# Kernel optimization log

Measured on AMD Instinct MI355X. Metric: run time of the kernel, lower is better.

## Reference

```python
import jax, jax.numpy as jnp
import numpy as np

N = 8192       # nodes
E = 131072     # edges
R = 4          # relations
IN_EMBD = 64   # per-feature embedding dim -> node feat = 6*64 = 384
H1 = 256       # layer_embd
D = 128        # out_embd; layer2 outputs 2*D
VOCABS = [35, 10, 5, 7, 5, 5]


def setup_inputs() -> dict:
    key = jax.random.key(0)
    ks = jax.random.split(key, 20)
    inp = {}
    inp['x'] = jax.random.randint(ks[0], (N, 6), 0, 5)
    inp['edge_index'] = jax.random.randint(ks[1], (2, E), 0, N)
    inp['edge_type'] = jax.random.randint(ks[2], (E,), 0, R)
    for i, v in enumerate(VOCABS):
        inp[f'emb{i}'] = jax.random.normal(ks[3 + i], (v, IN_EMBD), jnp.float32) * 0.1
    inp['W1'] = jax.random.normal(ks[10], (R, 6 * IN_EMBD, H1), jnp.float32) * 0.05
    inp['root1'] = jax.random.normal(ks[11], (6 * IN_EMBD, H1), jnp.float32) * 0.05
    inp['b1'] = jnp.zeros((H1,), jnp.float32)
    inp['W2'] = jax.random.normal(ks[12], (R, H1, 2 * D), jnp.float32) * 0.05
    inp['root2'] = jax.random.normal(ks[13], (H1, 2 * D), jnp.float32) * 0.05
    inp['b2'] = jnp.zeros((2 * D,), jnp.float32)
    return inp


def _rgcn(h, W, root, b, src, dst, edge_type):
    # RGCNConv (PyG semantics): out_i = root h_i + b + sum_r mean_{j in N_r(i)} W_r h_j
    out = h @ root + b
    for r in range(R):
        hr = h @ W[r]                                   # [N, out]
        m = (edge_type == r).astype(h.dtype)            # [E]
        s = jax.ops.segment_sum(hr[src] * m[:, None], dst, num_segments=N)
        c = jax.ops.segment_sum(m, dst, num_segments=N)
        out = out + s / jnp.clip(c, 1.0)[:, None]
    return out


def reference(x, edge_index, edge_type, emb0, emb1, emb2, emb3, emb4, emb5,
              W1, root1, b1, W2, root2, b2):
    embs = [emb0, emb1, emb2, emb3, emb4, emb5]
    x_ = jnp.concatenate([embs[i][x[:, i]] for i in range(6)], axis=1)  # [N, 384]
    src, dst = edge_index[0], edge_index[1]
    h1 = jax.nn.sigmoid(_rgcn(x_, W1, root1, b1, src, dst, edge_type))
    h2 = jax.nn.sigmoid(_rgcn(h1, W2, root2, b2, src, dst, edge_type))
    mu, logvar = h2[:, :D], h2[:, D:]
    std = jnp.exp(0.5 * logvar)
    eps = jax.random.normal(jax.random.key(42), std.shape, std.dtype)
    Z = eps * std + mu                                   # reparametrize
    A_hat = jax.nn.sigmoid(Z @ Z.T)                      # [N, N]
    A = jnp.zeros((N, N), jnp.float32).at[src, dst].set(1.0)
    return A, A_hat, mu, logvar
```

## Files before the change

### kernel.cpp

```cpp
#include <hip/hip_runtime.h>
#include <hip/hip_bf16.h>
#include <cstdint>
#include <cstddef>

#define N_NODES 8192
#define NE      131072
#define NR      4
#define NC      1280
#define SLOTS   96

typedef __attribute__((ext_vector_type(8))) short bf16x8;
typedef __attribute__((ext_vector_type(4))) float f32x4;

__device__ __forceinline__ float sigmoidf_(float x) {
  return 1.0f / (1.0f + __expf(-x));
}

__device__ __forceinline__ ushort f2b(float v) {
  __hip_bfloat16 h = __float2bfloat16(v);
  return *(ushort*)&h;
}
__device__ __forceinline__ float b2f(ushort u) {
  __hip_bfloat16 h = *(__hip_bfloat16*)&u;
  return __bfloat162float(h);
}
__device__ __forceinline__ void split2(float v, ushort& hi, ushort& lo) {
  hi = f2b(v);
  lo = f2b(v - b2f(hi));
}
__device__ __forceinline__ bf16x8 pack8(float4 a, float4 b) {
  bf16x8 r;
  r[0] = (short)f2b(a.x); r[1] = (short)f2b(a.y); r[2] = (short)f2b(a.z); r[3] = (short)f2b(a.w);
  r[4] = (short)f2b(b.x); r[5] = (short)f2b(b.y); r[6] = (short)f2b(b.z); r[7] = (short)f2b(b.w);
  return r;
}

__global__ __launch_bounds__(256) void k_pack_all(
    const float* __restrict__ r1, const float* __restrict__ W1,
    const float* __restrict__ r2, const float* __restrict__ W2,
    ushort* __restrict__ B1t, ushort* __restrict__ B2thi, ushort* __restrict__ B2tlo) {
  __shared__ ushort sh[64][66];
  __shared__ ushort sl[64][66];
  int b = blockIdx.x;
  int layer, K, kt, nt, seg;
  const float *srcR, *srcW;
  if (b < 120) { layer = 1; K = 384; int t = b;       seg = t / 24; t %= 24; kt = t / 4; nt = t % 4; srcR = r1; srcW = W1; }
  else         { layer = 2; K = 256; int t = b - 120; seg = t / 16; t %= 16; kt = t / 4; nt = t % 4; srcR = r2; srcW = W2; }
  int k0 = kt * 64, n0 = nt * 64;
  int tid = threadIdx.x;
#pragma unroll
  for (int it = 0; it < 16; ++it) {
    int idx = it * 256 + tid;
    int kl = idx >> 6, nl = idx & 63;
    int kg = k0 + kl, c = n0 + nl;
    float v = (seg == 0) ? srcR[(size_t)kg * 256 + c]
                         : srcW[((size_t)(seg - 1) * K + kg) * 256 + c];
    ushort h, l; split2(v, h, l);
    sh[kl][nl] = h;
    sl[kl][nl] = l;
  }
  __syncthreads();
#pragma unroll
  for (int it = 0; it < 16; ++it) {
    int idx = it * 256 + tid;
    int nl = idx >> 6, kl = idx & 63;
    size_t o = (size_t)(seg * 256 + n0 + nl) * K + k0 + kl;
    if (layer == 1) {
      B1t[o] = sh[kl][nl];
    } else {
      B2thi[o] = sh[kl][nl];
      B2tlo[o] = sl[kl][nl];
    }
  }
}

__global__ void k_fill2(const int* __restrict__ src, const int* __restrict__ dst,
                        const int* __restrict__ et,
                        int* __restrict__ cnt, int* __restrict__ slots,
                        int* __restrict__ cnt2, int* __restrict__ slots2) {
  int e = blockIdx.x * 256 + threadIdx.x;
  if (e < NE) {
    int d = dst[e], s = src[e];
    int pos = atomicAdd(&cnt[d], 1);
    if (pos < SLOTS) slots[(size_t)d * SLOTS + pos] = (s << 2) | et[e];
    int pos2 = atomicAdd(&cnt2[s], 1);
    if (pos2 < SLOTS) slots2[(size_t)s * SLOTS + pos2] = d;
  }
}

__global__ __launch_bounds__(256) void k_arow(const int* __restrict__ cnt2,
                                              const int* __restrict__ slots2,
                                              float* __restrict__ A) {
  __shared__ float row[N_NODES];
  int n = blockIdx.x, tid = threadIdx.x;
  float4 z = make_float4(0.f, 0.f, 0.f, 0.f);
#pragma unroll
  for (int it = 0; it < 8; ++it)
    *(float4*)&row[(it * 256 + tid) * 4] = z;
  __syncthreads();
  int m = min(cnt2[n], SLOTS);
  if (tid < m) row[slots2[(size_t)n * SLOTS + tid]] = 1.0f;
  __syncthreads();
  float4* out4 = (float4*)(A + (size_t)n * N_NODES);
#pragma unroll
  for (int it = 0; it < 8; ++it) {
    int i = it * 256 + tid;
    out4[i] = *(const float4*)&row[i * 4];
  }
}

__global__ __launch_bounds__(256) void k_gemm1e(
    const int* __restrict__ x,
    const float* __restrict__ e0, const float* __restrict__ e1,
    const float* __restrict__ e2, const float* __restrict__ e3,
    const float* __restrict__ e4, const float* __restrict__ e5,
    const ushort* __restrict__ Bhi, ushort* __restrict__ Cb) {
  constexpr int K = 384;
  __shared__ ushort BsH[128 * 128];
  const int tid = threadIdx.x;
  const int w = tid >> 6, l = tid & 63;
  const int lrow = l & 15, lk8 = (l >> 4) * 8;
  const int brow = blockIdx.y * 128, bcol = blockIdx.x * 128;
  const int r0 = brow + w * 32 + lrow, r1i = r0 + 16;

  int idx0[6], idx1[6];
#pragma unroll
  for (int j = 0; j < 3; ++j) {
    int2 a = *(const int2*)(x + (size_t)r0 * 6 + j * 2);
    idx0[j * 2] = a.x; idx0[j * 2 + 1] = a.y;
    int2 b = *(const int2*)(x + (size_t)r1i * 6 + j * 2);
    idx1[j * 2] = b.x; idx1[j * 2 + 1] = b.y;
  }
  const float* tabs[6] = {e0, e1, e2, e3, e4, e5};

  f32x4 acc[2][8] = {};
#pragma unroll
  for (int kc = 0; kc < K; kc += 128) {
    bf16x8 aH[4][2];
#pragma unroll
    for (int kk = 0; kk < 4; ++kk) {
      const int base = kc + kk * 32;
      const int ti = base >> 6;
      const int dd = (base & 63) + lk8;
      const float* t0 = tabs[ti] + (size_t)idx0[ti] * 64 + dd;
      const float* t1 = tabs[ti] + (size_t)idx1[ti] * 64 + dd;
      aH[kk][0] = pack8(*(const float4*)t0, *(const float4*)(t0 + 4));
      aH[kk][1] = pack8(*(const float4*)t1, *(const float4*)(t1 + 4));
    }
    if (kc) __syncthreads();
#pragma unroll
    for (int it = 0; it < 8; ++it) {
      int o = (it * 256 + tid) * 16;
      int row = o >> 8, sb = o & 255;
      int se = (sb ^ ((row & 7) << 4)) >> 1;
      size_t g = (size_t)(bcol + row) * K + kc + se;
      *(uint4*)((char*)BsH + o) = *(const uint4*)(Bhi + g);
    }
    __syncthreads();
#pragma unroll
    for (int kk = 0; kk < 4; ++kk) {
#pragma unroll
      for (int n = 0; n < 8; ++n) {
        int row_t = n * 16 + lrow;
        int addr = row_t * 256 + ((kk * 64 + (l >> 4) * 16) ^ ((row_t & 7) << 4));
        bf16x8 b_h = *(const bf16x8*)((const char*)BsH + addr);
        acc[0][n] = __builtin_amdgcn_mfma_f32_16x16x32_bf16(aH[kk][0], b_h, acc[0][n], 0, 0, 0);
        acc[1][n] = __builtin_amdgcn_mfma_f32_16x16x32_bf16(aH[kk][1], b_h, acc[1][n], 0, 0, 0);
      }
    }
  }
  const int crow = (l >> 4) * 4, ccol = l & 15;
#pragma unroll
  for (int m = 0; m < 2; ++m)
#pragma unroll
    for (int n = 0; n < 8; ++n) {
      int rloc = w * 32 + m * 16 + crow;
      int cloc = n * 16 + ccol;
#pragma unroll
      for (int r = 0; r < 4; ++r)
        Cb[(size_t)(brow + rloc + r) * NC + bcol + cloc] = f2b(acc[m][n][r]);
    }
}

template<int SPLIT3, int ACT, int SYM, int OUT>
__global__ __launch_bounds__(256) void k_gemm2(
    const ushort* __restrict__ Ahi, const ushort* __restrict__ Alo,
    const ushort* __restrict__ Bhi, const ushort* __restrict__ Blo,
    void* __restrict__ Cv, int Nc, int K) {
  __shared__ ushort Bs[(SPLIT3 ? 2 : 1) * 128 * 128];
  ushort* BsH = Bs;
  ushort* BsL = Bs + 128 * 128;

  const int tid = threadIdx.x;
  const int w = tid >> 6, l = tid & 63;
  const int lrow = l & 15, lk8 = (l >> 4) * 8;

  int brow, bcol, p = 0, q = 0;
  if (SYM) {
    int b = blockIdx.x;
    q = (int)((sqrtf(8.f * (float)b + 1.f) - 1.f) * 0.5f);
    while ((q + 1) * (q + 2) / 2 <= b) ++q;
    while (q * (q + 1) / 2 > b) --q;
    p = b - q * (q + 1) / 2;
    brow = p * 128; bcol = q * 128;
  } else {
    brow = blockIdx.y * 128; bcol = blockIdx.x * 128;
  }

  f32x4 acc[2][8] = {};
  const size_t arow0 = (size_t)(brow + w * 32 + lrow) * K + lk8;
  const size_t arow1 = arow0 + (size_t)16 * K;

  for (int kc = 0; kc < K; kc += 128) {
    bf16x8 aH[4][2], aL[4][2];
#pragma unroll
    for (int kk = 0; kk < 4; ++kk) {
      aH[kk][0] = *(const bf16x8*)(Ahi + arow0 + kc + kk * 32);
      aH[kk][1] = *(const bf16x8*)(Ahi + arow1 + kc + kk * 32);
      if (SPLIT3) {
        aL[kk][0] = *(const bf16x8*)(Alo + arow0 + kc + kk * 32);
        aL[kk][1] = *(const bf16x8*)(Alo + arow1 + kc + kk * 32);
      }
    }
    if (kc) __syncthreads();
#pragma unroll
    for (int it = 0; it < 8; ++it) {
      int o = (it * 256 + tid) * 16;
      int row = o >> 8, sb = o & 255;
      int se = (sb ^ ((row & 7) << 4)) >> 1;
      size_t g = (size_t)(bcol + row) * K + kc + se;
      *(uint4*)((char*)BsH + o) = *(const uint4*)(Bhi + g);
      if (SPLIT3) *(uint4*)((char*)BsL + o) = *(const uint4*)(Blo + g);
    }
    __syncthreads();
#pragma unroll
    for (int kk = 0; kk < 4; ++kk) {
#pragma unroll
      for (int n = 0; n < 8; ++n) {
        int row_t = n * 16 + lrow;
        int addr = row_t * 256 + ((kk * 64 + (l >> 4) * 16) ^ ((row_t & 7) << 4));
        bf16x8 b_h = *(const bf16x8*)((const char*)BsH + addr);
        acc[0][n] = __builtin_amdgcn_mfma_f32_16x16x32_bf16(aH[kk][0], b_h, acc[0][n], 0, 0, 0);
        acc[1][n] = __builtin_amdgcn_mfma_f32_16x16x32_bf16(aH[kk][1], b_h, acc[1][n], 0, 0, 0);
        if (SPLIT3) {
          bf16x8 b_l = *(const bf16x8*)((const char*)BsL + addr);
          acc[0][n] = __builtin_amdgcn_mfma_f32_16x16x32_bf16(aL[kk][0], b_h, acc[0][n], 0, 0, 0);
          acc[1][n] = __builtin_amdgcn_mfma_f32_16x16x32_bf16(aL[kk][1], b_h, acc[1][n], 0, 0, 0);
          acc[0][n] = __builtin_amdgcn_mfma_f32_16x16x32_bf16(aH[kk][0], b_l, acc[0][n], 0, 0, 0);
          acc[1][n] = __builtin_amdgcn_mfma_f32_16x16x32_bf16(aH[kk][1], b_l, acc[1][n], 0, 0, 0);
        }
      }
    }
  }

  const int crow = (l >> 4) * 4, ccol = l & 15;
  float*  Cf = (float*)Cv;
  ushort* Cb = (ushort*)Cv;
  const int domirror = (SYM && p != q);
  if (SYM) { if (domirror) __syncthreads(); }
  float* T = (float*)Bs;
#pragma unroll
  for (int m = 0; m < 2; ++m)
#pragma unroll
    for (int n = 0; n < 8; ++n) {
      float v[4];
#pragma unroll
      for (int r = 0; r < 4; ++r) {
        float t = acc[m][n][r];
        v[r] = ACT ? sigmoidf_(t) : t;
      }
      int rloc = w * 32 + m * 16 + crow;
      int cloc = n * 16 + ccol;
#pragma unroll
      for (int r = 0; r < 4; ++r) {
        if (OUT) Cb[(size_t)(brow + rloc + r) * Nc + bcol + cloc] = f2b(v[r]);
        else     Cf[(size_t)(brow + rloc + r) * Nc + bcol + cloc] = v[r];
      }
      if (SYM && p != q) {
        int s = (cloc & 7) << 2;
#pragma unroll
        for (int r = 0; r < 4; ++r) T[cloc * 128 + ((rloc + r) ^ s)] = v[r];
      }
    }
  if (SYM && p != q) {
    __syncthreads();
#pragma unroll
    for (int it = 0; it < 16; ++it) {
      int idx = it * 256 + tid;
      int rw = idx >> 5;
      int c4 = (idx & 31) * 4;
      int s = (rw & 7) << 2;
      float4 val = *(const float4*)&T[rw * 128 + (c4 ^ s)];
      *(float4*)(Cf + (size_t)(bcol + rw) * Nc + brow + c4) = val;
    }
  }
}

__device__ __forceinline__ float bits_to_normal(unsigned bits) {
  float f = __uint_as_float((bits >> 9) | 0x3f800000u) - 1.0f;
  const float lo = -0.99999994f;
  float u = __fadd_rn(__fmul_rn(f, 2.0f), lo);
  u = fmaxf(lo, u);
  float w = -log1pf(-u * u);
  float p;
  if (w < 5.0f) {
    w = w - 2.5f;
    p = 2.81022636e-08f;
    p = fmaf(p, w, 3.43273939e-07f);
    p = fmaf(p, w, -3.5233877e-06f);
    p = fmaf(p, w, -4.39150654e-06f);
    p = fmaf(p, w, 0.00021858087f);
    p = fmaf(p, w, -0.00125372503f);
    p = fmaf(p, w, -0.00417768164f);
    p = fmaf(p, w, 0.246640727f);
    p = fmaf(p, w, 1.50140941f);
  } else {
    w = sqrtf(w) - 3.0f;
    p = -0.000200214257f;
    p = fmaf(p, w, 0.000100950558f);
    p = fmaf(p, w, 0.00134934322f);
    p = fmaf(p, w, -0.00367342844f);
    p = fmaf(p, w, 0.00573950773f);
    p = fmaf(p, w, -0.0076224613f);
    p = fmaf(p, w, 0.00943887047f);
    p = fmaf(p, w, 1.00167406f);
    p = fmaf(p, w, 2.83297682f);
  }
  return 1.41421356f * (p * u);
}

__device__ __forceinline__ unsigned threefry_bits(unsigned j) {
  const unsigned ks0 = 0u, ks1 = 42u, ks2 = 0x1BD11BDAu ^ 0u ^ 42u;
  unsigned x0 = 0u + ks0;
  unsigned x1 = j + ks1;
#define RND(r) { x0 += x1; x1 = (x1 << r) | (x1 >> (32 - r)); x1 ^= x0; }
  RND(13) RND(15) RND(26) RND(6)  x0 += ks1; x1 += ks2 + 1u;
  RND(17) RND(29) RND(16) RND(24) x0 += ks2; x1 += ks0 + 2u;
  RND(13) RND(15) RND(26) RND(6)  x0 += ks0; x1 += ks1 + 3u;
  RND(17) RND(29) RND(16) RND(24) x0 += ks1; x1 += ks2 + 4u;
  RND(13) RND(15) RND(26) RND(6)  x0 += ks2; x1 += ks0 + 5u;
#undef RND
  return x0 ^ x1;
}

__global__ __launch_bounds__(256) void k_combine1(
    const ushort* __restrict__ hall, const float* __restrict__ bias,
    const int* __restrict__ cnt, const int* __restrict__ slots,
    ushort* __restrict__ h_hi, ushort* __restrict__ h_lo) {
  __shared__ int sc[64];
  int n = blockIdx.x, c = threadIdx.x;
  int end = min(cnt[n], SLOTS);
  const int* sl = slots + (size_t)n * SLOTS;
  float a0 = 0.f, a1 = 0.f, a2 = 0.f, a3 = 0.f;
  int c0 = 0, c1 = 0, c2 = 0, c3 = 0;
  for (int base = 0; base < end; base += 64) {
    int mcnt = min(64, end - base);
    if (c < 64 && base + c < end) sc[c] = sl[base + c];
    __syncthreads();
    int i = 0;
    for (; i + 4 <= mcnt; i += 4) {
      int p0 = sc[i], p1 = sc[i + 1], p2 = sc[i + 2], p3 = sc[i + 3];
      float v0 = b2f(hall[(size_t)(p0 >> 2) * NC + 256 + (size_t)(p0 & 3) * 256 + c]);
      float v1 = b2f(hall[(size_t)(p1 >> 2) * NC + 256 + (size_t)(p1 & 3) * 256 + c]);
      float v2 = b2f(hall[(size_t)(p2 >> 2) * NC + 256 + (size_t)(p2 & 3) * 256 + c]);
      float v3 = b2f(hall[(size_t)(p3 >> 2) * NC + 256 + (size_t)(p3 & 3) * 256 + c]);
      int r;
      r = p0 & 3; if (r == 0) { a0 += v0; ++c0; } else if (r == 1) { a1 += v0; ++c1; }
                  else if (r == 2) { a2 += v0; ++c2; } else { a3 += v0; ++c3; }
      r = p1 & 3; if (r == 0) { a0 += v1; ++c0; } else if (r == 1) { a1 += v1; ++c1; }
                  else if (r == 2) { a2 += v1; ++c2; } else { a3 += v1; ++c3; }
      r = p2 & 3; if (r == 0) { a0 += v2; ++c0; } else if (r == 1) { a1 += v2; ++c1; }
                  else if (r == 2) { a2 += v2; ++c2; } else { a3 += v2; ++c3; }
      r = p3 & 3; if (r == 0) { a0 += v3; ++c0; } else if (r == 1) { a1 += v3; ++c1; }
                  else if (r == 2) { a2 += v3; ++c2; } else { a3 += v3; ++c3; }
    }
    for (; i < mcnt; ++i) {
      int pp = sc[i];
      int r = pp & 3;
      float v = b2f(hall[(size_t)(pp >> 2) * NC + 256 + (size_t)r * 256 + c]);
      if (r == 0) { a0 += v; ++c0; } else if (r == 1) { a1 += v; ++c1; }
      else if (r == 2) { a2 += v; ++c2; } else { a3 += v; ++c3; }
    }
    __syncthreads();
  }
  float v = b2f(hall[(size_t)n * NC + c]) + bias[c]
          + a0 / (float)max(c0, 1) + a1 / (float)max(c1, 1)
          + a2 / (float)max(c2, 1) + a3 / (float)max(c3, 1);
  float sg = sigmoidf_(v);
  ushort h, l; split2(sg, h, l);
  h_hi[(size_t)n * 256 + c] = h;
  h_lo[(size_t)n * 256 + c] = l;
}

__global__ __launch_bounds__(256) void k_combine2z(
    const float* __restrict__ hall, const float* __restrict__ bias,
    const int* __restrict__ cnt, const int* __restrict__ slots,
    float* __restrict__ muo, float* __restrict__ lvo,
    ushort* __restrict__ zhi, ushort* __restrict__ zlo) {
  __shared__ int sc[64];
  __shared__ float sv[256];
  int n = blockIdx.x, c = threadIdx.x;
  int end = min(cnt[n], SLOTS);
  const int* sl = slots + (size_t)n * SLOTS;
  float a0 = 0.f, a1 = 0.f, a2 = 0.f, a3 = 0.f;
  int c0 = 0, c1 = 0, c2 = 0, c3 = 0;
  for (int base = 0; base < end; base += 64) {
    int mcnt = min(64, end - base);
    if (c < 64 && base + c < end) sc[c] = sl[base + c];
    __syncthreads();
    int i = 0;
    for (; i + 4 <= mcnt; i += 4) {
      int p0 = sc[i], p1 = sc[i + 1], p2 = sc[i + 2], p3 = sc[i + 3];
      float v0 = hall[(size_t)(p0 >> 2) * NC + 256 + (size_t)(p0 & 3) * 256 + c];
      float v1 = hall[(size_t)(p1 >> 2) * NC + 256 + (size_t)(p1 & 3) * 256 + c];
      float v2 = hall[(size_t)(p2 >> 2) * NC + 256 + (size_t)(p2 & 3) * 256 + c];
      float v3 = hall[(size_t)(p3 >> 2) * NC + 256 + (size_t)(p3 & 3) * 256 + c];
      int r;
      r = p0 & 3; if (r == 0) { a0 += v0; ++c0; } else if (r == 1) { a1 += v0; ++c1; }
                  else if (r == 2) { a2 += v0; ++c2; } else { a3 += v0; ++c3; }
      r = p1 & 3; if (r == 0) { a0 += v1; ++c0; } else if (r == 1) { a1 += v1; ++c1; }
                  else if (r == 2) { a2 += v1; ++c2; } else { a3 += v1; ++c3; }
      r = p2 & 3; if (r == 0) { a0 += v2; ++c0; } else if (r == 1) { a1 += v2; ++c1; }
                  else if (r == 2) { a2 += v2; ++c2; } else { a3 += v2; ++c3; }
      r = p3 & 3; if (r == 0) { a0 += v3; ++c0; } else if (r == 1) { a1 += v3; ++c1; }
                  else if (r == 2) { a2 += v3; ++c2; } else { a3 += v3; ++c3; }
    }
    for (; i < mcnt; ++i) {
      int pp = sc[i];
      int r = pp & 3;
      float v = hall[(size_t)(pp >> 2) * NC + 256 + (size_t)r * 256 + c];
      if (r == 0) { a0 += v; ++c0; } else if (r == 1) { a1 += v; ++c1; }
      else if (r == 2) { a2 += v; ++c2; } else { a3 += v; ++c3; }
    }
    __syncthreads();
  }
  float v = hall[(size_t)n * NC + c] + bias[c]
          + a0 / (float)max(c0, 1) + a1 / (float)max(c1, 1)
          + a2 / (float)max(c2, 1) + a3 / (float)max(c3, 1);
  float sg = sigmoidf_(v);
  if (c < 128) muo[(size_t)n * 128 + c] = sg;
  else         lvo[(size_t)n * 128 + (c - 128)] = sg;
  sv[c] = sg;
  __syncthreads();
  if (c < 128) {
    unsigned j = (unsigned)n * 128u + (unsigned)c;
    float e = bits_to_normal(threefry_bits(j));
    float z = fmaf(e, __expf(0.5f * sv[c + 128]), sv[c]);
    ushort h, l; split2(z, h, l);
    zhi[j] = h; zlo[j] = l;
  }
}

extern "C" void kernel_launch(void* const* d_in, const int* in_sizes, int n_in,
                              void* d_out, int out_size, void* d_ws, size_t ws_size,
                              hipStream_t stream) {
  const int* x    = (const int*)d_in[0];
  const int* ei   = (const int*)d_in[1];
  const int* src  = ei;
  const int* dst  = ei + NE;
  const int* et   = (const int*)d_in[2];
  const float* e0 = (const float*)d_in[3];
  const float* e1 = (const float*)d_in[4];
  const float* e2 = (const float*)d_in[5];
  const float* e3 = (const float*)d_in[6];
  const float* e4 = (const float*)d_in[7];
  const float* e5 = (const float*)d_in[8];
  const float* W1 = (const float*)d_in[9];
  const float* r1 = (const float*)d_in[10];
  const float* b1 = (const float*)d_in[11];
  const float* W2 = (const float*)d_in[12];
  const float* r2 = (const float*)d_in[13];
  const float* b2 = (const float*)d_in[14];

  float* out  = (float*)d_out;
  float* A    = out;
  float* Ahat = out + (size_t)N_NODES * N_NODES;
  float* muo  = Ahat + (size_t)N_NODES * N_NODES;
  float* lvo  = muo + (size_t)N_NODES * 128;

  char* wp = (char*)d_ws;
  auto carve = [&](size_t bytes) { char* r = wp; wp += (bytes + 255) & ~(size_t)255; return r; };
  ushort* B1t    = (ushort*)carve((size_t)NC * 384 * 2);
  ushort* B2thi  = (ushort*)carve((size_t)NC * 256 * 2);
  ushort* B2tlo  = (ushort*)carve((size_t)NC * 256 * 2);
  float*  hall   = (float*)carve((size_t)8192 * NC * 4);
  ushort* hallb  = (ushort*)hall;
  ushort* h1hi   = (ushort*)carve((size_t)8192 * 256 * 2);
  ushort* h1lo   = (ushort*)carve((size_t)8192 * 256 * 2);
  ushort* zhi    = (ushort*)carve((size_t)8192 * 128 * 2);
  ushort* zlo    = (ushort*)carve((size_t)8192 * 128 * 2);
  int*    cnt    = (int*)carve((size_t)8192 * 4);
  int*    cnt2   = (int*)carve((size_t)8192 * 4);
  int*    slots  = (int*)carve((size_t)8192 * SLOTS * 4);
  int*    slots2 = (int*)carve((size_t)8192 * SLOTS * 4);

  hipMemsetAsync(cnt, 0, (size_t)2 * 8192 * 4, stream);
  k_fill2<<<NE / 256, 256, 0, stream>>>(src, dst, et, cnt, slots, cnt2, slots2);

  k_arow<<<8192, 256, 0, stream>>>(cnt2, slots2, A);

  k_pack_all<<<200, 256, 0, stream>>>(r1, W1, r2, W2, B1t, B2thi, B2tlo);

  k_gemm1e<<<dim3(NC / 128, 64), 256, 0, stream>>>(
      x, e0, e1, e2, e3, e4, e5, B1t, hallb);
  k_combine1<<<8192, 256, 0, stream>>>(hallb, b1, cnt, slots, h1hi, h1lo);

  k_gemm2<1, 0, 0, 0><<<dim3(NC / 128, 64), 256, 0, stream>>>(
      h1hi, h1lo, B2thi, B2tlo, hall, NC, 256);
  k_combine2z<<<8192, 256, 0, stream>>>(hall, b2, cnt, slots, muo, lvo, zhi, zlo);

  k_gemm2<1, 1, 1, 0><<<dim3(64 * 65 / 2), 256, 0, stream>>>(
      zhi, zlo, zhi, zlo, Ahat, N_NODES, 128);
}
```

Measured before the change: 295.2 us.

## Fuse edge fill with weight packing and adjacency rows into combine1

Merges the edge-slot fill kernel and the weight pack kernel into one launch by splitting the grid on block index. Moves dense adjacency-row writing into the layer-1 combine kernel as extra blocks, and rewrites it to build a per-thread 32-bit mask by scanning the slot list instead of zeroing a shared-memory row. This removes two launches and lets the bandwidth-bound A write overlap with the gather-bound combine. The mask scan makes every thread loop over all of a node's edges, and the added branches may raise register pressure in the combine kernel.

```diff
diff --git a/kernel.cpp b/kernel.cpp
--- a/kernel.cpp
+++ b/kernel.cpp
@@ -35,13 +35,25 @@
   return r;
 }
 
-__global__ __launch_bounds__(256) void k_pack_all(
+__global__ __launch_bounds__(256) void k_fill_pack(
+    const int* __restrict__ src, const int* __restrict__ dst, const int* __restrict__ et,
+    int* __restrict__ cnt, int* __restrict__ slots,
+    int* __restrict__ cnt2, int* __restrict__ slots2,
     const float* __restrict__ r1, const float* __restrict__ W1,
     const float* __restrict__ r2, const float* __restrict__ W2,
     ushort* __restrict__ B1t, ushort* __restrict__ B2thi, ushort* __restrict__ B2tlo) {
   __shared__ ushort sh[64][66];
   __shared__ ushort sl[64][66];
-  int b = blockIdx.x;
+  if (blockIdx.x < 512) {
+    int e = blockIdx.x * 256 + threadIdx.x;
+    int d = dst[e], s = src[e];
+    int pos = atomicAdd(&cnt[d], 1);
+    if (pos < SLOTS) slots[(size_t)d * SLOTS + pos] = (s << 2) | et[e];
+    int pos2 = atomicAdd(&cnt2[s], 1);
+    if (pos2 < SLOTS) slots2[(size_t)s * SLOTS + pos2] = d;
+    return;
+  }
+  int b = blockIdx.x - 512;
   int layer, K, kt, nt, seg;
   const float *srcR, *srcW;
   if (b < 120) { layer = 1; K = 384; int t = b;       seg = t / 24; t %= 24; kt = t / 4; nt = t % 4; srcR = r1; srcW = W1; }
@@ -71,41 +83,6 @@
       B2thi[o] = sh[kl][nl];
       B2tlo[o] = sl[kl][nl];
     }
-  }
-}
-
-__global__ void k_fill2(const int* __restrict__ src, const int* __restrict__ dst,
-                        const int* __restrict__ et,
-                        int* __restrict__ cnt, int* __restrict__ slots,
-                        int* __restrict__ cnt2, int* __restrict__ slots2) {
-  int e = blockIdx.x * 256 + threadIdx.x;
-  if (e < NE) {
-    int d = dst[e], s = src[e];
-    int pos = atomicAdd(&cnt[d], 1);
-    if (pos < SLOTS) slots[(size_t)d * SLOTS + pos] = (s << 2) | et[e];
-    int pos2 = atomicAdd(&cnt2[s], 1);
-    if (pos2 < SLOTS) slots2[(size_t)s * SLOTS + pos2] = d;
-  }
-}
-
-__global__ __launch_bounds__(256) void k_arow(const int* __restrict__ cnt2,
-                                              const int* __restrict__ slots2,
-                                              float* __restrict__ A) {
-  __shared__ float row[N_NODES];
-  int n = blockIdx.x, tid = threadIdx.x;
-  float4 z = make_float4(0.f, 0.f, 0.f, 0.f);
-#pragma unroll
-  for (int it = 0; it < 8; ++it)
-    *(float4*)&row[(it * 256 + tid) * 4] = z;
-  __syncthreads();
-  int m = min(cnt2[n], SLOTS);
-  if (tid < m) row[slots2[(size_t)n * SLOTS + tid]] = 1.0f;
-  __syncthreads();
-  float4* out4 = (float4*)(A + (size_t)n * N_NODES);
-#pragma unroll
-  for (int it = 0; it < 8; ++it) {
-    int i = it * 256 + tid;
-    out4[i] = *(const float4*)&row[i * 4];
   }
 }
 
@@ -343,11 +320,35 @@
   return x0 ^ x1;
 }
 
-__global__ __launch_bounds__(256) void k_combine1(
+__global__ __launch_bounds__(256) void k_combine1A(
     const ushort* __restrict__ hall, const float* __restrict__ bias,
     const int* __restrict__ cnt, const int* __restrict__ slots,
-    ushort* __restrict__ h_hi, ushort* __restrict__ h_lo) {
+    ushort* __restrict__ h_hi, ushort* __restrict__ h_lo,
+    const int* __restrict__ cnt2, const int* __restrict__ slots2,
+    float* __restrict__ A) {
   __shared__ int sc[64];
+  if (blockIdx.x >= N_NODES) {
+    int n = blockIdx.x - N_NODES;
+    int tid = threadIdx.x;
+    int m = min(cnt2[n], SLOTS);
+    const int* sl2 = slots2 + (size_t)n * SLOTS;
+    unsigned mask = 0;
+    for (int j = 0; j < m; ++j) {
+      int d = sl2[j];
+      if ((d >> 5) == tid) mask |= 1u << (d & 31);
+    }
+    float* rowp = A + (size_t)n * N_NODES + tid * 32;
+#pragma unroll
+    for (int w2 = 0; w2 < 8; ++w2) {
+      float4 v;
+      v.x = (mask >> (w2 * 4 + 0)) & 1 ? 1.0f : 0.0f;
+      v.y = (mask >> (w2 * 4 + 1)) & 1 ? 1.0f : 0.0f;
+      v.z = (mask >> (w2 * 4 + 2)) & 1 ? 1.0f : 0.0f;
+      v.w = (mask >> (w2 * 4 + 3)) & 1 ? 1.0f : 0.0f;
+      *(float4*)(rowp + w2 * 4) = v;
+    }
+    return;
+  }
   int n = blockIdx.x, c = threadIdx.x;
   int end = min(cnt[n], SLOTS);
   const int* sl = slots + (size_t)n * SLOTS;
@@ -495,15 +496,14 @@
   int*    slots2 = (int*)carve((size_t)8192 * SLOTS * 4);
 
   hipMemsetAsync(cnt, 0, (size_t)2 * 8192 * 4, stream);
-  k_fill2<<<NE / 256, 256, 0, stream>>>(src, dst, et, cnt, slots, cnt2, slots2);
-
-  k_arow<<<8192, 256, 0, stream>>>(cnt2, slots2, A);
-
-  k_pack_all<<<200, 256, 0, stream>>>(r1, W1, r2, W2, B1t, B2thi, B2tlo);
+  k_fill_pack<<<712, 256, 0, stream>>>(src, dst, et, cnt, slots, cnt2, slots2,
+                                       r1, W1, r2, W2, B1t, B2thi, B2tlo);
 
   k_gemm1e<<<dim3(NC / 128, 64), 256, 0, stream>>>(
       x, e0, e1, e2, e3, e4, e5, B1t, hallb);
-  k_combine1<<<8192, 256, 0, stream>>>(hallb, b1, cnt, slots, h1hi, h1lo);
+
+  k_combine1A<<<2 * N_NODES, 256, 0, stream>>>(hallb, b1, cnt, slots, h1hi, h1lo,
+                                               cnt2, slots2, A);
 
   k_gemm2<1, 0, 0, 0><<<dim3(NC / 128, 64), 256, 0, stream>>>(
       h1hi, h1lo, B2thi, B2tlo, hall, NC, 256);
```

Measured after the change: 315.6 us. +6.9%, slower.
